# Kernel tuning notes

Hardware: AMD Instinct MI355X
Metric: run time of the kernel (lower is better)

The kernel has to match this reference:

```python
import jax, jax.numpy as jnp
import numpy as np

N = 50000            # nodes
E = 800000           # random edges (self loops added in reference, per PyG default)
D_IN, D1, D2, D_OUT = 256, 128, 64, 40
SLOPE = 0.2          # GATv2Conv default negative_slope


def _glorot(key, shape):
    fan_in, fan_out = shape[0], shape[-1]
    s = jnp.sqrt(6.0 / (fan_in + fan_out))
    return jax.random.uniform(key, shape, jnp.float32, -s, s)


def setup_inputs() -> dict:
    key = jax.random.key(0)
    ks = jax.random.split(key, 16)
    inp = {
        "x": jax.random.normal(ks[0], (N, D_IN), jnp.float32),
        "edge_index": jax.random.randint(ks[1], (2, E), 0, N),
    }
    dims = [(D_IN, D1), (D1, D2), (D2, D_OUT)]
    k = 2
    for i, (di, do) in enumerate(dims, 1):
        inp[f"W{i}l"] = _glorot(ks[k], (di, do)); k += 1
        inp[f"W{i}r"] = _glorot(ks[k], (di, do)); k += 1
        inp[f"b{i}l"] = jnp.zeros((do,), jnp.float32)
        inp[f"b{i}r"] = jnp.zeros((do,), jnp.float32)
        inp[f"a{i}"]  = _glorot(ks[k], (do,));    k += 1
        inp[f"c{i}"]  = jnp.zeros((do,), jnp.float32)
    return inp


def _gatv2(x, src, dst, Wl, bl, Wr, br, att, bias):
    # GATv2Conv, heads=1: lin_l on source nodes, lin_r on target nodes
    xl = x @ Wl + bl                     # [N, do] source transform
    xr = x @ Wr + br                     # [N, do] target transform
    e = jax.nn.leaky_relu(xl[src] + xr[dst], SLOPE)   # [Etot, do]
    logits = e @ att                     # [Etot]
    # segment softmax over incoming edges of each dst node
    m = jax.ops.segment_max(logits, dst, num_segments=N)
    ex = jnp.exp(logits - m[dst])
    denom = jax.ops.segment_sum(ex, dst, num_segments=N)
    alpha = ex / denom[dst]              # [Etot]
    out = jax.ops.segment_sum(alpha[:, None] * xl[src], dst, num_segments=N)
    return out + bias


def reference(x, edge_index,
              W1l, W1r, b1l, b1r, a1, c1,
              W2l, W2r, b2l, b2r, a2, c2,
              W3l, W3r, b3l, b3r, a3, c3):
    loop = jnp.arange(N, dtype=edge_index.dtype)
    src = jnp.concatenate([edge_index[0], loop])   # add_self_loops=True
    dst = jnp.concatenate([edge_index[1], loop])
    h = jax.nn.relu(_gatv2(x, src, dst, W1l, b1l, W1r, b1r, a1, c1))
    h = jax.nn.relu(_gatv2(h, src, dst, W2l, b2l, W2r, b2r, a2, c2))
    h = _gatv2(h, src, dst, W3l, b3l, W3r, b3r, a3, c3)
    return jax.nn.log_softmax(h, axis=1)
```

## Files before the change

### kernel.cpp

```cpp
#include <hip/hip_runtime.h>
#include <math.h>

#define NN 50000
#define NE 800000
#define SLOPE 0.2f
#define NEGX (-1e30f)
#define CH 8192

typedef _Float16 h8 __attribute__((ext_vector_type(8)));
typedef _Float16 h2 __attribute__((ext_vector_type(2)));
typedef float f8 __attribute__((ext_vector_type(8)));
typedef float v4f __attribute__((ext_vector_type(4)));

__device__ __forceinline__ h8 hzero(){ h8 z = {0,0,0,0,0,0,0,0}; return z; }

__device__ __forceinline__ void pack_one(const float* __restrict__ W,
                                         _Float16* __restrict__ Wp,
                                         int DO, int K, int NT, int t){
  int KC = K >> 5;
  if (t >= NT * KC * 64) return;
  int lane = t & 63;
  int rest = t >> 6;
  int c  = rest % KC;
  int nt = rest / KC;
  int col = nt * 16 + (lane & 15);
  int k0  = c * 32 + ((lane >> 4) << 3);
  _Float16 o[8];
#pragma unroll
  for (int j = 0; j < 8; j++){
    float v = (col < DO) ? W[(k0 + j) * DO + col] : 0.f;
    o[j] = (_Float16)v;
  }
  *(ulonglong2*)(Wp + (size_t)t * 8) = *(ulonglong2*)o;
}

__global__ __launch_bounds__(256) void k_pack_hist(
    const float* W1l, const float* W1r, const float* W2l,
    const float* W2r, const float* W3l, const float* W3r,
    _Float16* p1l, _Float16* p1r, _Float16* p2l,
    _Float16* p2r, _Float16* p3l, _Float16* p3r,
    const int* __restrict__ ei, int* __restrict__ gbp){
  __shared__ int h[256];
  int b = blockIdx.x, t = threadIdx.x;
  if (b < 44){
    if      (b < 16) pack_one(W1l, p1l, 128, 256, 8, (b     ) * 256 + t);
    else if (b < 32) pack_one(W1r, p1r, 128, 256, 8, (b - 16) * 256 + t);
    else if (b < 36) pack_one(W2l, p2l,  64, 128, 4, (b - 32) * 256 + t);
    else if (b < 40) pack_one(W2r, p2r,  64, 128, 4, (b - 36) * 256 + t);
    else if (b < 42) pack_one(W3l, p3l,  40,  64, 3, (b - 40) * 256 + t);
    else             pack_one(W3r, p3r,  40,  64, 3, (b - 42) * 256 + t);
  } else {
    int hb = b - 44;
    h[t] = 0;
    __syncthreads();
    int e0 = hb * 12500;
    for (int i = t; i < 12500; i += 256)
      atomicAdd(&h[ei[NE + e0 + i] >> 8], 1);
    __syncthreads();
    gbp[hb * 256 + t] = h[t];
  }
}

__global__ __launch_bounds__(256) void k_scan(const int* __restrict__ gbp,
                                              int* __restrict__ base,
                                              int* __restrict__ bcur,
                                              int* __restrict__ row_ptr){
  __shared__ int s[256];
  int t = threadIdx.x;
  int v = 0;
#pragma unroll 8
  for (int i = 0; i < 64; i++) v += gbp[i * 256 + t];
  s[t] = v; __syncthreads();
  for (int off = 1; off < 256; off <<= 1){
    int a = (t >= off) ? s[t - off] : 0;
    __syncthreads(); s[t] += a; __syncthreads();
  }
  int ex = s[t] - v;
  base[t] = ex;
  bcur[t] = ex;
  if (t == 255){ base[256] = s[255]; row_ptr[NN] = s[255]; }
}

__global__ __launch_bounds__(256) void k_bscatter(const int* __restrict__ ei,
                                                  int* __restrict__ bcur,
                                                  unsigned* __restrict__ pk_out){
  __shared__ unsigned pk[CH];
  __shared__ int h[256];
  int t = threadIdx.x;
  int e0 = blockIdx.x * CH;
  h[t] = 0;
  __syncthreads();
  int n = NE - e0; if (n > CH) n = CH;
  for (int i = t; i < n; i += 256){
    int e = e0 + i;
    int s = ei[e], d = ei[NE + e];
    pk[i] = (unsigned)s | ((unsigned)(d & 255) << 16) | ((unsigned)(d >> 8) << 24);
    atomicAdd(&h[d >> 8], 1);
  }
  __syncthreads();
  int c = h[t];
  if (c) h[t] = atomicAdd(&bcur[t], c);
  __syncthreads();
  for (int i = t; i < n; i += 256){
    unsigned u = pk[i];
    int pos = atomicAdd(&h[u >> 24], 1);
    pk_out[pos] = u;
  }
}

__global__ __launch_bounds__(256) void k_bcsr(const unsigned* __restrict__ pk,
                                              const int* __restrict__ base,
                                              int* __restrict__ row_ptr,
                                              int* __restrict__ csr_src){
  __shared__ int h[256], s[256];
  int t = threadIdx.x;
  int b = blockIdx.x;
  int lo = base[b], hi = base[b + 1];
  h[t] = 0;
  __syncthreads();
  for (int i = lo + t; i < hi; i += 256)
    atomicAdd(&h[(pk[i] >> 16) & 255], 1);
  __syncthreads();
  int v = h[t];
  s[t] = v; __syncthreads();
  for (int off = 1; off < 256; off <<= 1){
    int a = (t >= off) ? s[t - off] : 0;
    __syncthreads(); s[t] += a; __syncthreads();
  }
  int ex = lo + s[t] - v;
  int node = b * 256 + t;
  if (node < NN) row_ptr[node] = ex;
  h[t] = ex;
  __syncthreads();
  for (int i = lo + t; i < hi; i += 256){
    unsigned u = pk[i];
    int pos = atomicAdd(&h[(u >> 16) & 255], 1);
    csr_src[pos] = (int)(u & 0xFFFFu);
  }
}

template<typename TI, int K, int DO>
__global__ __launch_bounds__(256, 4) void gemm_direct(
    const TI* __restrict__ X,
    const _Float16* __restrict__ Wpl, const float* __restrict__ bl,
    const _Float16* __restrict__ Wpr, const float* __restrict__ br,
    _Float16* __restrict__ Yl, _Float16* __restrict__ Yr)
{
  constexpr int KC = K / 32;
  constexpr int NT = (DO + 15) / 16;
  int lane = threadIdx.x & 63;
  int wv   = threadIdx.x >> 6;
  int row0 = (blockIdx.x * 4 + wv) * 16;
  int arow = lane & 15;
  int koff = lane >> 4;
  int lrow = row0 + arow;
  int crow = (lrow < NN) ? lrow : 0;

  h8 afrag[KC];
  if constexpr (sizeof(TI) == 4){
    const float* Xr = (const float*)X + (size_t)crow * K + koff * 8;
#pragma unroll
    for (int c = 0; c < KC; c++){
      float4 v0 = *reinterpret_cast<const float4*>(Xr + c * 32);
      float4 v1 = *reinterpret_cast<const float4*>(Xr + c * 32 + 4);
      h8 a;
      a[0]=(_Float16)v0.x; a[1]=(_Float16)v0.y; a[2]=(_Float16)v0.z; a[3]=(_Float16)v0.w;
      a[4]=(_Float16)v1.x; a[5]=(_Float16)v1.y; a[6]=(_Float16)v1.z; a[7]=(_Float16)v1.w;
      afrag[c] = a;
    }
  } else {
    const _Float16* Xr = (const _Float16*)X + (size_t)crow * K + koff * 8;
#pragma unroll
    for (int c = 0; c < KC; c++)
      afrag[c] = *reinterpret_cast<const h8*>(Xr + c * 32);
  }

#pragma unroll
  for (int side = 0; side < 2; side++){
    const _Float16* Wp = side ? Wpr : Wpl;
    const float* bias = side ? br : bl;
    _Float16* Y = side ? Yr : Yl;
#pragma unroll
    for (int nt = 0; nt < NT; nt++){
      v4f acc = {0.f, 0.f, 0.f, 0.f};
#pragma unroll
      for (int c = 0; c < KC; c++){
        h8 b = *reinterpret_cast<const h8*>(Wp + (size_t)((nt * KC + c) * 64 + lane) * 8);
        acc = __builtin_amdgcn_mfma_f32_16x16x32_f16(afrag[c], b, acc, 0, 0, 0);
      }
      int col = nt * 16 + arow;
      if (col < DO){
        float bv = bias[col];
        int rbase = row0 + koff * 4;
#pragma unroll
        for (int r = 0; r < 4; r++){
          int orow = rbase + r;
          if (orow < NN) Y[(size_t)orow * DO + col] = (_Float16)(acc[r] + bv);
        }
      }
    }
  }
}

__device__ __forceinline__ float edge_logit(h8 x, h8 xrv, h8 attv){
  h8 t = x + xrv;
  h8 l = __builtin_elementwise_max(t, t * (_Float16)SLOPE);
  const h2* lp = (const h2*)&l;
  const h2* ap = (const h2*)&attv;
  h2 d = lp[0] * ap[0];
  d += lp[1] * ap[1];
  d += lp[2] * ap[2];
  d += lp[3] * ap[3];
  return (float)d[0] + (float)d[1];
}

template<int LPG>
__device__ __forceinline__ float gsum(float v){
#pragma unroll
  for (int off = 1; off < LPG; off <<= 1) v += __shfl_xor(v, off, 64);
  return v;
}
template<int LPG>
__device__ __forceinline__ void gsum2(float& a, float& b){
#pragma unroll
  for (int off = 1; off < LPG; off <<= 1){
    a += __shfl_xor(a, off, 64);
    b += __shfl_xor(b, off, 64);
  }
}
template<int LPG>
__device__ __forceinline__ float gmax(float v){
#pragma unroll
  for (int off = 1; off < LPG; off <<= 1) v = fmaxf(v, __shfl_xor(v, off, 64));
  return v;
}

template<int DO, int LPG, int DO2>
__global__ __launch_bounds__(256) void agg_gemm(
    const _Float16* __restrict__ xl, const _Float16* __restrict__ xr,
    const int* __restrict__ csr_src, const int* __restrict__ row_ptr,
    const float* __restrict__ att, const float* __restrict__ bias,
    const _Float16* __restrict__ Wpl2, const float* __restrict__ bl2,
    const _Float16* __restrict__ Wpr2, const float* __restrict__ br2,
    _Float16* __restrict__ Yl, _Float16* __restrict__ Yr)
{
  constexpr int G = 64 / LPG;
  constexpr int NPB = 4 * G;
  constexpr int LK = DO + 8;
  constexpr int KC2 = DO / 32;
  constexpr int NT2 = (DO2 + 15) / 16;
  constexpr int MT = NPB / 16;
  __shared__ _Float16 hs[NPB * LK];

  int lane = threadIdx.x & 63;
  int wid  = threadIdx.x >> 6;
  int g = lane / LPG, p = lane % LPG;
  int nodeLocal = wid * G + g;
  int node = blockIdx.x * NPB + nodeLocal;
  int cbase = p * 8;
  bool nvalid = node < NN;
  int nodeC = nvalid ? node : 0;

  h8 attv, xrv, xlv;
  {
    float4 a0 = *reinterpret_cast<const float4*>(att + cbase);
    float4 a1 = *reinterpret_cast<const float4*>(att + cbase + 4);
    attv[0]=(_Float16)a0.x; attv[1]=(_Float16)a0.y; attv[2]=(_Float16)a0.z; attv[3]=(_Float16)a0.w;
    attv[4]=(_Float16)a1.x; attv[5]=(_Float16)a1.y; attv[6]=(_Float16)a1.z; attv[7]=(_Float16)a1.w;
    xrv = *reinterpret_cast<const h8*>(xr + nodeC * DO + cbase);
    xlv = *reinterpret_cast<const h8*>(xl + nodeC * DO + cbase);
  }
  float s = gsum<LPG>(edge_logit(xlv, xrv, attv));
  float wS = __expf(s);
  float denA = wS, denB = 0.f;
  float accA[8], accB[8];
  {
    f8 xf = __builtin_convertvector(xlv, f8);
#pragma unroll
    for (int j = 0; j < 8; j++){ accA[j] = wS * xf[j]; accB[j] = 0.f; }
  }

  int e0 = row_ptr[nodeC];
  int e1 = nvalid ? row_ptr[nodeC + 1] : e0;
  int e = e0;
  for (; e + 1 < e1; e += 2){
    int sA = csr_src[e], sB = csr_src[e + 1];
    h8 xA = *reinterpret_cast<const h8*>(xl + sA * DO + cbase);
    h8 xB = *reinterpret_cast<const h8*>(xl + sB * DO + cbase);
    float pA = edge_logit(xA, xrv, attv);
    float pB = edge_logit(xB, xrv, attv);
    gsum2<LPG>(pA, pB);
    float wA = __expf(pA), wB = __expf(pB);
    denA += wA; denB += wB;
    f8 fA = __builtin_convertvector(xA, f8);
    f8 fB = __builtin_convertvector(xB, f8);
#pragma unroll
    for (int j = 0; j < 8; j++){
      accA[j] = fmaf(wA, fA[j], accA[j]);
      accB[j] = fmaf(wB, fB[j], accB[j]);
    }
  }
  if (e < e1){
    int sA = csr_src[e];
    h8 xA = *reinterpret_cast<const h8*>(xl + sA * DO + cbase);
    float pA = gsum<LPG>(edge_logit(xA, xrv, attv));
    float w = __expf(pA);
    denA += w;
    f8 fA = __builtin_convertvector(xA, f8);
#pragma unroll
    for (int j = 0; j < 8; j++) accA[j] = fmaf(w, fA[j], accA[j]);
  }

  {
    float inv = 1.0f / (denA + denB);
    f8 vv;
#pragma unroll
    for (int j = 0; j < 8; j++)
      vv[j] = fmaxf(fmaf(accA[j] + accB[j], inv, bias[cbase + j]), 0.f);
    h8 ho = __builtin_convertvector(vv, h8);
    *reinterpret_cast<h8*>(&hs[nodeLocal * LK + cbase]) = ho;
  }
  __syncthreads();

  int arow = lane & 15;
  int koff = lane >> 4;
  int mt = (MT == 1) ? 0 : (wid >> 1);
  h8 afrag[KC2];
#pragma unroll
  for (int c = 0; c < KC2; c++)
    afrag[c] = *reinterpret_cast<const h8*>(&hs[(mt * 16 + arow) * LK + koff * 8 + c * 32]);

  int row0 = blockIdx.x * NPB + mt * 16;
  int side = wid & 1;
  const _Float16* Wp = side ? Wpr2 : Wpl2;
  const float* bias2 = side ? br2 : bl2;
  _Float16* Y = side ? Yr : Yl;
  int nt_begin = (MT == 1) ? (wid >> 1) * (NT2 / 2) : 0;
  int nt_end   = (MT == 1) ? nt_begin + NT2 / 2 : NT2;
  for (int nt = nt_begin; nt < nt_end; nt++){
    v4f acc = {0.f, 0.f, 0.f, 0.f};
#pragma unroll
    for (int c = 0; c < KC2; c++){
      h8 b = *reinterpret_cast<const h8*>(Wp + (size_t)((nt * KC2 + c) * 64 + lane) * 8);
      acc = __builtin_amdgcn_mfma_f32_16x16x32_f16(afrag[c], b, acc, 0, 0, 0);
    }
    int col = nt * 16 + arow;
    if (col < DO2){
      float bv = bias2[col];
      int rbase = row0 + koff * 4;
#pragma unroll
      for (int r = 0; r < 4; r++){
        int orow = rbase + r;
        if (orow < NN) Y[(size_t)orow * DO2 + col] = (_Float16)(acc[r] + bv);
      }
    }
  }
}

template<int DO, int LPG>
__global__ __launch_bounds__(256) void gat_agg_out(
    const _Float16* __restrict__ xl, const _Float16* __restrict__ xr,
    const int* __restrict__ csr_src, const int* __restrict__ row_ptr,
    const float* __restrict__ att, const float* __restrict__ bias,
    float* __restrict__ out)
{
  constexpr int G = 64 / LPG;
  int lane = threadIdx.x & 63;
  int wv = (blockIdx.x * 256 + threadIdx.x) >> 6;
  int g = lane / LPG;
  int p = lane % LPG;
  int node = wv * G + g;
  if (node >= NN) return;
  int cbase = p * 8;
  bool ok = (cbase < DO);

  h8 attv = hzero(), xrv = hzero(), xlv = hzero();
  if (ok){
    float4 a0 = *reinterpret_cast<const float4*>(att + cbase);
    float4 a1 = *reinterpret_cast<const float4*>(att + cbase + 4);
    attv[0]=(_Float16)a0.x; attv[1]=(_Float16)a0.y; attv[2]=(_Float16)a0.z; attv[3]=(_Float16)a0.w;
    attv[4]=(_Float16)a1.x; attv[5]=(_Float16)a1.y; attv[6]=(_Float16)a1.z; attv[7]=(_Float16)a1.w;
    xrv = *reinterpret_cast<const h8*>(xr + node * DO + cbase);
    xlv = *reinterpret_cast<const h8*>(xl + node * DO + cbase);
  }

  float s = gsum<LPG>(edge_logit(xlv, xrv, attv));
  float wS = __expf(s);
  float denA = wS, denB = 0.f;
  float accA[8], accB[8];
  {
    f8 xf = __builtin_convertvector(xlv, f8);
#pragma unroll
    for (int j = 0; j < 8; j++){ accA[j] = wS * xf[j]; accB[j] = 0.f; }
  }

  int e0 = row_ptr[node], e1 = row_ptr[node + 1];
  int e = e0;
  for (; e + 1 < e1; e += 2){
    int sA = csr_src[e], sB = csr_src[e + 1];
    h8 xA = ok ? *reinterpret_cast<const h8*>(xl + sA * DO + cbase) : hzero();
    h8 xB = ok ? *reinterpret_cast<const h8*>(xl + sB * DO + cbase) : hzero();
    float pA = edge_logit(xA, xrv, attv);
    float pB = edge_logit(xB, xrv, attv);
    gsum2<LPG>(pA, pB);
    float wA = __expf(pA), wB = __expf(pB);
    denA += wA; denB += wB;
    f8 fA = __builtin_convertvector(xA, f8);
    f8 fB = __builtin_convertvector(xB, f8);
#pragma unroll
    for (int j = 0; j < 8; j++){
      accA[j] = fmaf(wA, fA[j], accA[j]);
      accB[j] = fmaf(wB, fB[j], accB[j]);
    }
  }
  if (e < e1){
    int sA = csr_src[e];
    h8 xA = ok ? *reinterpret_cast<const h8*>(xl + sA * DO + cbase) : hzero();
    float pA = gsum<LPG>(edge_logit(xA, xrv, attv));
    float w = __expf(pA);
    denA += w;
    f8 fA = __builtin_convertvector(xA, f8);
#pragma unroll
    for (int j = 0; j < 8; j++) accA[j] = fmaf(w, fA[j], accA[j]);
  }

  float inv = 1.0f / (denA + denB);
  float v[8]; float lmax = NEGX;
#pragma unroll
  for (int j = 0; j < 8; j++){
    v[j] = ok ? fmaf(accA[j] + accB[j], inv, bias[cbase + j]) : NEGX;
    lmax = fmaxf(lmax, v[j]);
  }
  lmax = gmax<LPG>(lmax);
  float lsum = 0.f;
#pragma unroll
  for (int j = 0; j < 8; j++) lsum += __expf(v[j] - lmax);
  lsum = gsum<LPG>(lsum);
  if (ok){
    float lg = lmax + __logf(lsum);
    float* op = (float*)out + node * DO + cbase;
    float4 o0, o1;
    o0.x = v[0] - lg; o0.y = v[1] - lg; o0.z = v[2] - lg; o0.w = v[3] - lg;
    o1.x = v[4] - lg; o1.y = v[5] - lg; o1.z = v[6] - lg; o1.w = v[7] - lg;
    *reinterpret_cast<float4*>(op) = o0;
    *reinterpret_cast<float4*>(op + 4) = o1;
  }
}

extern "C" void kernel_launch(void* const* d_in, const int* in_sizes, int n_in,
                              void* d_out, int out_size, void* d_ws, size_t ws_size,
                              hipStream_t stream) {
  const float* x   = (const float*)d_in[0];
  const int*   ei  = (const int*)d_in[1];
  const float* W1l = (const float*)d_in[2];  const float* W1r = (const float*)d_in[3];
  const float* b1l = (const float*)d_in[4];  const float* b1r = (const float*)d_in[5];
  const float* a1  = (const float*)d_in[6];  const float* c1  = (const float*)d_in[7];
  const float* W2l = (const float*)d_in[8];  const float* W2r = (const float*)d_in[9];
  const float* b2l = (const float*)d_in[10]; const float* b2r = (const float*)d_in[11];
  const float* a2  = (const float*)d_in[12]; const float* c2  = (const float*)d_in[13];
  const float* W3l = (const float*)d_in[14]; const float* W3r = (const float*)d_in[15];
  const float* b3l = (const float*)d_in[16]; const float* b3r = (const float*)d_in[17];
  const float* a3  = (const float*)d_in[18]; const float* c3  = (const float*)d_in[19];
  float* outp = (float*)d_out;

  _Float16* xl1 = (_Float16*)d_ws;
  _Float16* xr1 = xl1 + 6400000;
  _Float16* xl2 = xr1 + 6400000;
  _Float16* xr2 = xl2 + 3200000;
  _Float16* xl3 = xr2 + 3200000;
  _Float16* xr3 = xl3 + 2000000;
  _Float16* wp1l = xr3 + 2000000;
  _Float16* wp1r = wp1l + 32768;
  _Float16* wp2l = wp1r + 32768;
  _Float16* wp2r = wp2l + 8192;
  _Float16* wp3l = wp2r + 8192;
  _Float16* wp3r = wp3l + 3072;
  unsigned* pk   = (unsigned*)(wp3r + 3072);
  int* csr_src   = (int*)(pk + NE);
  int* row_ptr   = csr_src + NE;
  int* gbp       = row_ptr + 50001;
  int* base      = gbp + 16384;
  int* bcur      = base + 257;

  const int GB = (NN + 63) / 64;
  const int SB = (NE + CH - 1) / CH;
  const int FB1 = (NN + 15) / 16;
  const int FB2 = (NN + 31) / 32;
  const int AB3 = (NN + 31) / 32;

  k_pack_hist<<<108, 256, 0, stream>>>(W1l, W1r, W2l, W2r, W3l, W3r,
                                       wp1l, wp1r, wp2l, wp2r, wp3l, wp3r,
                                       ei, gbp);
  k_scan<<<1, 256, 0, stream>>>(gbp, base, bcur, row_ptr);
  k_bscatter<<<SB, 256, 0, stream>>>(ei, bcur, pk);
  k_bcsr<<<196, 256, 0, stream>>>(pk, base, row_ptr, csr_src);

  gemm_direct<float,256,128><<<GB, 256, 0, stream>>>(x, wp1l, b1l, wp1r, b1r, xl1, xr1);

  agg_gemm<128,16,64><<<FB1, 256, 0, stream>>>(xl1, xr1, csr_src, row_ptr,
                                               a1, c1, wp2l, b2l, wp2r, b2r, xl2, xr2);

  agg_gemm<64,8,40><<<FB2, 256, 0, stream>>>(xl2, xr2, csr_src, row_ptr,
                                             a2, c2, wp3l, b3l, wp3r, b3r, xl3, xr3);

  gat_agg_out<40,8><<<AB3, 256, 0, stream>>>(xl3, xr3, csr_src, row_ptr, a3, c3, outp);
}
```

Baseline: 285.6 us.

## Sort nodes by degree within each block and unroll edge loop by four

Each block now computes its nodes' in-degrees, ranks them in shared memory, and assigns nodes to wave groups in degree order, so the groups within a wave have similar edge counts and less divergence. The GEMM epilogue writes rows through the resulting permutation. The edge loop gains a 4-way unrolled path with batched shuffle reductions to keep more gathers in flight, and the accumulators become vector types. It costs extra syncthreads, an O(NPB^2) ranking step and scattered row writes.

```diff
diff --git a/kernel.cpp b/kernel.cpp
--- a/kernel.cpp
+++ b/kernel.cpp
@@ -13,6 +13,7 @@
 typedef float v4f __attribute__((ext_vector_type(4)));
 
 __device__ __forceinline__ h8 hzero(){ h8 z = {0,0,0,0,0,0,0,0}; return z; }
+__device__ __forceinline__ f8 fzero(){ f8 z = {0,0,0,0,0,0,0,0}; return z; }
 
 __device__ __forceinline__ void pack_one(const float* __restrict__ W,
                                          _Float16* __restrict__ Wp,
@@ -229,6 +230,16 @@
   }
 }
 template<int LPG>
+__device__ __forceinline__ void gsum4(float& a, float& b, float& c, float& d){
+#pragma unroll
+  for (int off = 1; off < LPG; off <<= 1){
+    a += __shfl_xor(a, off, 64);
+    b += __shfl_xor(b, off, 64);
+    c += __shfl_xor(c, off, 64);
+    d += __shfl_xor(d, off, 64);
+  }
+}
+template<int LPG>
 __device__ __forceinline__ float gmax(float v){
 #pragma unroll
   for (int off = 1; off < LPG; off <<= 1) v = fmaxf(v, __shfl_xor(v, off, 64));
@@ -251,12 +262,33 @@
   constexpr int NT2 = (DO2 + 15) / 16;
   constexpr int MT = NPB / 16;
   __shared__ _Float16 hs[NPB * LK];
-
-  int lane = threadIdx.x & 63;
-  int wid  = threadIdx.x >> 6;
+  __shared__ int nodeOf[NPB];
+  __shared__ int degOf[NPB];
+
+  int tid  = threadIdx.x;
+  int lane = tid & 63;
+  int wid  = tid >> 6;
+
+  if (tid < NPB){
+    int nd = blockIdx.x * NPB + tid;
+    degOf[tid] = (nd < NN) ? (row_ptr[nd + 1] - row_ptr[nd]) : -1;
+  }
+  __syncthreads();
+  if (tid < NPB){
+    int dg = degOf[tid];
+    int r = 0;
+#pragma unroll
+    for (int j = 0; j < NPB; j++){
+      int dj = degOf[j];
+      r += (dj < dg) || (dj == dg && j < tid);
+    }
+    nodeOf[r] = blockIdx.x * NPB + tid;
+  }
+  __syncthreads();
+
   int g = lane / LPG, p = lane % LPG;
   int nodeLocal = wid * G + g;
-  int node = blockIdx.x * NPB + nodeLocal;
+  int node = nodeOf[nodeLocal];
   int cbase = p * 8;
   bool nvalid = node < NN;
   int nodeC = nvalid ? node : 0;
@@ -273,16 +305,36 @@
   float s = gsum<LPG>(edge_logit(xlv, xrv, attv));
   float wS = __expf(s);
   float denA = wS, denB = 0.f;
-  float accA[8], accB[8];
+  f8 accA, accB;
   {
     f8 xf = __builtin_convertvector(xlv, f8);
-#pragma unroll
-    for (int j = 0; j < 8; j++){ accA[j] = wS * xf[j]; accB[j] = 0.f; }
+    accA = xf * wS;
+    accB = fzero();
   }
 
   int e0 = row_ptr[nodeC];
   int e1 = nvalid ? row_ptr[nodeC + 1] : e0;
   int e = e0;
+  for (; e + 3 < e1; e += 4){
+    int s0 = csr_src[e],     s1 = csr_src[e + 1];
+    int s2 = csr_src[e + 2], s3 = csr_src[e + 3];
+    h8 x0 = *reinterpret_cast<const h8*>(xl + s0 * DO + cbase);
+    h8 x1 = *reinterpret_cast<const h8*>(xl + s1 * DO + cbase);
+    h8 x2 = *reinterpret_cast<const h8*>(xl + s2 * DO + cbase);
+    h8 x3 = *reinterpret_cast<const h8*>(xl + s3 * DO + cbase);
+    float p0 = edge_logit(x0, xrv, attv);
+    float p1 = edge_logit(x1, xrv, attv);
+    float p2 = edge_logit(x2, xrv, attv);
+    float p3 = edge_logit(x3, xrv, attv);
+    gsum4<LPG>(p0, p1, p2, p3);
+    float w0 = __expf(p0), w1 = __expf(p1);
+    float w2 = __expf(p2), w3 = __expf(p3);
+    denA += w0 + w2; denB += w1 + w3;
+    accA = __builtin_convertvector(x0, f8) * w0 + accA;
+    accB = __builtin_convertvector(x1, f8) * w1 + accB;
+    accA = __builtin_convertvector(x2, f8) * w2 + accA;
+    accB = __builtin_convertvector(x3, f8) * w3 + accB;
+  }
   for (; e + 1 < e1; e += 2){
     int sA = csr_src[e], sB = csr_src[e + 1];
     h8 xA = *reinterpret_cast<const h8*>(xl + sA * DO + cbase);
@@ -292,13 +344,8 @@
     gsum2<LPG>(pA, pB);
     float wA = __expf(pA), wB = __expf(pB);
     denA += wA; denB += wB;
-    f8 fA = __builtin_convertvector(xA, f8);
-    f8 fB = __builtin_convertvector(xB, f8);
-#pragma unroll
-    for (int j = 0; j < 8; j++){
-      accA[j] = fmaf(wA, fA[j], accA[j]);
-      accB[j] = fmaf(wB, fB[j], accB[j]);
-    }
+    accA = __builtin_convertvector(xA, f8) * wA + accA;
+    accB = __builtin_convertvector(xB, f8) * wB + accB;
   }
   if (e < e1){
     int sA = csr_src[e];
@@ -306,19 +353,18 @@
     float pA = gsum<LPG>(edge_logit(xA, xrv, attv));
     float w = __expf(pA);
     denA += w;
-    f8 fA = __builtin_convertvector(xA, f8);
-#pragma unroll
-    for (int j = 0; j < 8; j++) accA[j] = fmaf(w, fA[j], accA[j]);
+    accA = __builtin_convertvector(xA, f8) * w + accA;
   }
 
   {
     float inv = 1.0f / (denA + denB);
-    f8 vv;
-#pragma unroll
-    for (int j = 0; j < 8; j++)
-      vv[j] = fmaxf(fmaf(accA[j] + accB[j], inv, bias[cbase + j]), 0.f);
-    h8 ho = __builtin_convertvector(vv, h8);
-    *reinterpret_cast<h8*>(&hs[nodeLocal * LK + cbase]) = ho;
+    f8 sum = (accA + accB) * inv;
+    float4 b0 = *reinterpret_cast<const float4*>(bias + cbase);
+    float4 b1 = *reinterpret_cast<const float4*>(bias + cbase + 4);
+    f8 bv = {b0.x, b0.y, b0.z, b0.w, b1.x, b1.y, b1.z, b1.w};
+    sum += bv;
+    sum = __builtin_elementwise_max(sum, fzero());
+    *reinterpret_cast<h8*>(&hs[nodeLocal * LK + cbase]) = __builtin_convertvector(sum, h8);
   }
   __syncthreads();
 
@@ -330,7 +376,6 @@
   for (int c = 0; c < KC2; c++)
     afrag[c] = *reinterpret_cast<const h8*>(&hs[(mt * 16 + arow) * LK + koff * 8 + c * 32]);
 
-  int row0 = blockIdx.x * NPB + mt * 16;
   int side = wid & 1;
   const _Float16* Wp = side ? Wpr2 : Wpl2;
   const float* bias2 = side ? br2 : bl2;
@@ -347,10 +392,10 @@
     int col = nt * 16 + arow;
     if (col < DO2){
       float bv = bias2[col];
-      int rbase = row0 + koff * 4;
+      int lrbase = mt * 16 + koff * 4;
 #pragma unroll
       for (int r = 0; r < 4; r++){
-        int orow = rbase + r;
+        int orow = nodeOf[lrbase + r];
         if (orow < NN) Y[(size_t)orow * DO2 + col] = (_Float16)(acc[r] + bv);
       }
     }
@@ -365,12 +410,35 @@
     float* __restrict__ out)
 {
   constexpr int G = 64 / LPG;
-  int lane = threadIdx.x & 63;
-  int wv = (blockIdx.x * 256 + threadIdx.x) >> 6;
+  constexpr int NPB = 4 * G;
+  __shared__ int nodeOf[NPB];
+  __shared__ int degOf[NPB];
+  int tid  = threadIdx.x;
+  int lane = tid & 63;
+  int wid  = tid >> 6;
+
+  if (tid < NPB){
+    int nd = blockIdx.x * NPB + tid;
+    degOf[tid] = (nd < NN) ? (row_ptr[nd + 1] - row_ptr[nd]) : -1;
+  }
+  __syncthreads();
+  if (tid < NPB){
+    int dg = degOf[tid];
+    int r = 0;
+#pragma unroll
+    for (int j = 0; j < NPB; j++){
+      int dj = degOf[j];
+      r += (dj < dg) || (dj == dg && j < tid);
+    }
+    nodeOf[r] = blockIdx.x * NPB + tid;
+  }
+  __syncthreads();
+
   int g = lane / LPG;
   int p = lane % LPG;
-  int node = wv * G + g;
-  if (node >= NN) return;
+  int node = nodeOf[wid * G + g];
+  bool nvalid = node < NN;
+  int nodeC = nvalid ? node : 0;
   int cbase = p * 8;
   bool ok = (cbase < DO);
 
@@ -380,22 +448,43 @@
     float4 a1 = *reinterpret_cast<const float4*>(att + cbase + 4);
     attv[0]=(_Float16)a0.x; attv[1]=(_Float16)a0.y; attv[2]=(_Float16)a0.z; attv[3]=(_Float16)a0.w;
     attv[4]=(_Float16)a1.x; attv[5]=(_Float16)a1.y; attv[6]=(_Float16)a1.z; attv[7]=(_Float16)a1.w;
-    xrv = *reinterpret_cast<const h8*>(xr + node * DO + cbase);
-    xlv = *reinterpret_cast<const h8*>(xl + node * DO + cbase);
+    xrv = *reinterpret_cast<const h8*>(xr + nodeC * DO + cbase);
+    xlv = *reinterpret_cast<const h8*>(xl + nodeC * DO + cbase);
   }
 
   float s = gsum<LPG>(edge_logit(xlv, xrv, attv));
   float wS = __expf(s);
   float denA = wS, denB = 0.f;
-  float accA[8], accB[8];
+  f8 accA, accB;
   {
     f8 xf = __builtin_convertvector(xlv, f8);
-#pragma unroll
-    for (int j = 0; j < 8; j++){ accA[j] = wS * xf[j]; accB[j] = 0.f; }
-  }
-
-  int e0 = row_ptr[node], e1 = row_ptr[node + 1];
+    accA = xf * wS;
+    accB = fzero();
+  }
+
+  int e0 = row_ptr[nodeC];
+  int e1 = nvalid ? row_ptr[nodeC + 1] : e0;
   int e = e0;
+  for (; e + 3 < e1; e += 4){
+    int s0 = csr_src[e],     s1 = csr_src[e + 1];
+    int s2 = csr_src[e + 2], s3 = csr_src[e + 3];
+    h8 x0 = ok ? *reinterpret_cast<const h8*>(xl + s0 * DO + cbase) : hzero();
+    h8 x1 = ok ? *reinterpret_cast<const h8*>(xl + s1 * DO + cbase) : hzero();
+    h8 x2 = ok ? *reinterpret_cast<const h8*>(xl + s2 * DO + cbase) : hzero();
+    h8 x3 = ok ? *reinterpret_cast<const h8*>(xl + s3 * DO + cbase) : hzero();
+    float p0 = edge_logit(x0, xrv, attv);
+    float p1 = edge_logit(x1, xrv, attv);
+    float p2 = edge_logit(x2, xrv, attv);
+    float p3 = edge_logit(x3, xrv, attv);
+    gsum4<LPG>(p0, p1, p2, p3);
+    float w0 = __expf(p0), w1 = __expf(p1);
+    float w2 = __expf(p2), w3 = __expf(p3);
+    denA += w0 + w2; denB += w1 + w3;
+    accA = __builtin_convertvector(x0, f8) * w0 + accA;
+    accB = __builtin_convertvector(x1, f8) * w1 + accB;
+    accA = __builtin_convertvector(x2, f8) * w2 + accA;
+    accB = __builtin_convertvector(x3, f8) * w3 + accB;
+  }
   for (; e + 1 < e1; e += 2){
     int sA = csr_src[e], sB = csr_src[e + 1];
     h8 xA = ok ? *reinterpret_cast<const h8*>(xl + sA * DO + cbase) : hzero();
@@ -405,13 +494,8 @@
     gsum2<LPG>(pA, pB);
     float wA = __expf(pA), wB = __expf(pB);
     denA += wA; denB += wB;
-    f8 fA = __builtin_convertvector(xA, f8);
-    f8 fB = __builtin_convertvector(xB, f8);
-#pragma unroll
-    for (int j = 0; j < 8; j++){
-      accA[j] = fmaf(wA, fA[j], accA[j]);
-      accB[j] = fmaf(wB, fB[j], accB[j]);
-    }
+    accA = __builtin_convertvector(xA, f8) * wA + accA;
+    accB = __builtin_convertvector(xB, f8) * wB + accB;
   }
   if (e < e1){
     int sA = csr_src[e];
@@ -419,16 +503,15 @@
     float pA = gsum<LPG>(edge_logit(xA, xrv, attv));
     float w = __expf(pA);
     denA += w;
-    f8 fA = __builtin_convertvector(xA, f8);
-#pragma unroll
-    for (int j = 0; j < 8; j++) accA[j] = fmaf(w, fA[j], accA[j]);
+    accA = __builtin_convertvector(xA, f8) * w + accA;
   }
 
   float inv = 1.0f / (denA + denB);
+  f8 sumv = (accA + accB) * inv;
   float v[8]; float lmax = NEGX;
 #pragma unroll
   for (int j = 0; j < 8; j++){
-    v[j] = ok ? fmaf(accA[j] + accB[j], inv, bias[cbase + j]) : NEGX;
+    v[j] = ok ? (sumv[j] + bias[cbase + j]) : NEGX;
     lmax = fmaxf(lmax, v[j]);
   }
   lmax = gmax<LPG>(lmax);
@@ -436,7 +519,7 @@
 #pragma unroll
   for (int j = 0; j < 8; j++) lsum += __expf(v[j] - lmax);
   lsum = gsum<LPG>(lsum);
-  if (ok){
+  if (ok && nvalid){
     float lg = lmax + __logf(lsum);
     float* op = (float*)out + node * DO + cbase;
     float4 o0, o1;
```

After: 290.1 us. Within noise of the previous version (+1.6%).

## Software-pipeline edge gathers in 4-edge batches with index prefetch

Applied to the files above, without the earlier changes.

Restructures the per-node edge aggregation loop in both aggregation kernels to process four edges per step. It prefetches the next batch's feature rows and the following batch's CSR indices while the current batch is being computed, using masked clamped indices instead of remainder handling. The goal is to raise memory-level parallelism on the irregular gathers and hide their latency. It also adds a launch-bounds occupancy hint and vectorises the accumulators and bias epilogue. The deeper pipeline raises register pressure, and short-degree nodes do wasted work on masked lanes.

```diff
diff --git a/kernel.cpp b/kernel.cpp
--- a/kernel.cpp
+++ b/kernel.cpp
@@ -13,6 +13,7 @@
 typedef float v4f __attribute__((ext_vector_type(4)));
 
 __device__ __forceinline__ h8 hzero(){ h8 z = {0,0,0,0,0,0,0,0}; return z; }
+__device__ __forceinline__ f8 fzero(){ f8 z = {0,0,0,0,0,0,0,0}; return z; }
 
 __device__ __forceinline__ void pack_one(const float* __restrict__ W,
                                          _Float16* __restrict__ Wp,
@@ -221,11 +222,13 @@
   return v;
 }
 template<int LPG>
-__device__ __forceinline__ void gsum2(float& a, float& b){
+__device__ __forceinline__ void gsum4(float& a, float& b, float& c, float& d){
 #pragma unroll
   for (int off = 1; off < LPG; off <<= 1){
     a += __shfl_xor(a, off, 64);
     b += __shfl_xor(b, off, 64);
+    c += __shfl_xor(c, off, 64);
+    d += __shfl_xor(d, off, 64);
   }
 }
 template<int LPG>
@@ -236,7 +239,7 @@
 }
 
 template<int DO, int LPG, int DO2>
-__global__ __launch_bounds__(256) void agg_gemm(
+__global__ __launch_bounds__(256, 4) void agg_gemm(
     const _Float16* __restrict__ xl, const _Float16* __restrict__ xr,
     const int* __restrict__ csr_src, const int* __restrict__ row_ptr,
     const float* __restrict__ att, const float* __restrict__ bias,
@@ -273,52 +276,84 @@
   float s = gsum<LPG>(edge_logit(xlv, xrv, attv));
   float wS = __expf(s);
   float denA = wS, denB = 0.f;
-  float accA[8], accB[8];
+  f8 accA, accB;
   {
     f8 xf = __builtin_convertvector(xlv, f8);
-#pragma unroll
-    for (int j = 0; j < 8; j++){ accA[j] = wS * xf[j]; accB[j] = 0.f; }
+    accA = xf * wS;
+    accB = fzero();
   }
 
   int e0 = row_ptr[nodeC];
   int e1 = nvalid ? row_ptr[nodeC + 1] : e0;
-  int e = e0;
-  for (; e + 1 < e1; e += 2){
-    int sA = csr_src[e], sB = csr_src[e + 1];
-    h8 xA = *reinterpret_cast<const h8*>(xl + sA * DO + cbase);
-    h8 xB = *reinterpret_cast<const h8*>(xl + sB * DO + cbase);
-    float pA = edge_logit(xA, xrv, attv);
-    float pB = edge_logit(xB, xrv, attv);
-    gsum2<LPG>(pA, pB);
-    float wA = __expf(pA), wB = __expf(pB);
-    denA += wA; denB += wB;
-    f8 fA = __builtin_convertvector(xA, f8);
-    f8 fB = __builtin_convertvector(xB, f8);
-#pragma unroll
-    for (int j = 0; j < 8; j++){
-      accA[j] = fmaf(wA, fA[j], accA[j]);
-      accB[j] = fmaf(wB, fB[j], accB[j]);
-    }
-  }
-  if (e < e1){
-    int sA = csr_src[e];
-    h8 xA = *reinterpret_cast<const h8*>(xl + sA * DO + cbase);
-    float pA = gsum<LPG>(edge_logit(xA, xrv, attv));
-    float w = __expf(pA);
-    denA += w;
-    f8 fA = __builtin_convertvector(xA, f8);
-#pragma unroll
-    for (int j = 0; j < 8; j++) accA[j] = fmaf(w, fA[j], accA[j]);
+  int deg = e1 - e0;
+  int clampE = (deg > 0) ? e1 - 1 : 0;
+
+  if (deg > 0){
+    int ic[4]; float vc[4]; h8 xc[4];
+#pragma unroll
+    for (int k = 0; k < 4; k++){
+      int ee = e0 + k; bool v = ee < e1;
+      ic[k] = csr_src[v ? ee : clampE]; vc[k] = v ? 1.f : 0.f;
+    }
+#pragma unroll
+    for (int k = 0; k < 4; k++)
+      xc[k] = *reinterpret_cast<const h8*>(xl + ic[k] * DO + cbase);
+    int in_[4]; float vn[4];
+    if (deg > 4){
+#pragma unroll
+      for (int k = 0; k < 4; k++){
+        int ee = e0 + 4 + k; bool v = ee < e1;
+        in_[k] = csr_src[v ? ee : clampE]; vn[k] = v ? 1.f : 0.f;
+      }
+    }
+    int i = 0;
+    while (true){
+      bool more = (i + 4 < deg);
+      h8 xn[4];
+      if (more){
+#pragma unroll
+        for (int k = 0; k < 4; k++)
+          xn[k] = *reinterpret_cast<const h8*>(xl + in_[k] * DO + cbase);
+      }
+      bool more2 = (i + 8 < deg);
+      int i2[4]; float v2[4];
+      if (more2){
+#pragma unroll
+        for (int k = 0; k < 4; k++){
+          int ee = e0 + i + 8 + k; bool v = ee < e1;
+          i2[k] = csr_src[v ? ee : clampE]; v2[k] = v ? 1.f : 0.f;
+        }
+      }
+      float p0 = edge_logit(xc[0], xrv, attv);
+      float p1 = edge_logit(xc[1], xrv, attv);
+      float p2 = edge_logit(xc[2], xrv, attv);
+      float p3 = edge_logit(xc[3], xrv, attv);
+      gsum4<LPG>(p0, p1, p2, p3);
+      float w0 = __expf(p0) * vc[0], w1 = __expf(p1) * vc[1];
+      float w2 = __expf(p2) * vc[2], w3 = __expf(p3) * vc[3];
+      denA += w0 + w2; denB += w1 + w3;
+      accA = __builtin_convertvector(xc[0], f8) * w0 + accA;
+      accB = __builtin_convertvector(xc[1], f8) * w1 + accB;
+      accA = __builtin_convertvector(xc[2], f8) * w2 + accA;
+      accB = __builtin_convertvector(xc[3], f8) * w3 + accB;
+      if (!more) break;
+#pragma unroll
+      for (int k = 0; k < 4; k++){
+        xc[k] = xn[k]; vc[k] = vn[k]; in_[k] = i2[k]; vn[k] = v2[k];
+      }
+      i += 4;
+    }
   }
 
   {
     float inv = 1.0f / (denA + denB);
-    f8 vv;
-#pragma unroll
-    for (int j = 0; j < 8; j++)
-      vv[j] = fmaxf(fmaf(accA[j] + accB[j], inv, bias[cbase + j]), 0.f);
-    h8 ho = __builtin_convertvector(vv, h8);
-    *reinterpret_cast<h8*>(&hs[nodeLocal * LK + cbase]) = ho;
+    f8 sum = (accA + accB) * inv;
+    float4 b0 = *reinterpret_cast<const float4*>(bias + cbase);
+    float4 b1 = *reinterpret_cast<const float4*>(bias + cbase + 4);
+    f8 bv = {b0.x, b0.y, b0.z, b0.w, b1.x, b1.y, b1.z, b1.w};
+    sum += bv;
+    sum = __builtin_elementwise_max(sum, fzero());
+    *reinterpret_cast<h8*>(&hs[nodeLocal * LK + cbase]) = __builtin_convertvector(sum, h8);
   }
   __syncthreads();
 
@@ -358,7 +393,7 @@
 }
 
 template<int DO, int LPG>
-__global__ __launch_bounds__(256) void gat_agg_out(
+__global__ __launch_bounds__(256, 4) void gat_agg_out(
     const _Float16* __restrict__ xl, const _Float16* __restrict__ xr,
     const int* __restrict__ csr_src, const int* __restrict__ row_ptr,
     const float* __restrict__ att, const float* __restrict__ bias,
@@ -387,48 +422,80 @@
   float s = gsum<LPG>(edge_logit(xlv, xrv, attv));
   float wS = __expf(s);
   float denA = wS, denB = 0.f;
-  float accA[8], accB[8];
+  f8 accA, accB;
   {
     f8 xf = __builtin_convertvector(xlv, f8);
-#pragma unroll
-    for (int j = 0; j < 8; j++){ accA[j] = wS * xf[j]; accB[j] = 0.f; }
+    accA = xf * wS;
+    accB = fzero();
   }
 
   int e0 = row_ptr[node], e1 = row_ptr[node + 1];
-  int e = e0;
-  for (; e + 1 < e1; e += 2){
-    int sA = csr_src[e], sB = csr_src[e + 1];
-    h8 xA = ok ? *reinterpret_cast<const h8*>(xl + sA * DO + cbase) : hzero();
-    h8 xB = ok ? *reinterpret_cast<const h8*>(xl + sB * DO + cbase) : hzero();
-    float pA = edge_logit(xA, xrv, attv);
-    float pB = edge_logit(xB, xrv, attv);
-    gsum2<LPG>(pA, pB);
-    float wA = __expf(pA), wB = __expf(pB);
-    denA += wA; denB += wB;
-    f8 fA = __builtin_convertvector(xA, f8);
-    f8 fB = __builtin_convertvector(xB, f8);
-#pragma unroll
-    for (int j = 0; j < 8; j++){
-      accA[j] = fmaf(wA, fA[j], accA[j]);
-      accB[j] = fmaf(wB, fB[j], accB[j]);
-    }
-  }
-  if (e < e1){
-    int sA = csr_src[e];
-    h8 xA = ok ? *reinterpret_cast<const h8*>(xl + sA * DO + cbase) : hzero();
-    float pA = gsum<LPG>(edge_logit(xA, xrv, attv));
-    float w = __expf(pA);
-    denA += w;
-    f8 fA = __builtin_convertvector(xA, f8);
-#pragma unroll
-    for (int j = 0; j < 8; j++) accA[j] = fmaf(w, fA[j], accA[j]);
+  int deg = e1 - e0;
+  int clampE = (deg > 0) ? e1 - 1 : 0;
+
+  if (deg > 0){
+    int ic[4]; float vc[4]; h8 xc[4];
+#pragma unroll
+    for (int k = 0; k < 4; k++){
+      int ee = e0 + k; bool v = ee < e1;
+      ic[k] = csr_src[v ? ee : clampE]; vc[k] = v ? 1.f : 0.f;
+    }
+#pragma unroll
+    for (int k = 0; k < 4; k++)
+      xc[k] = ok ? *reinterpret_cast<const h8*>(xl + ic[k] * DO + cbase) : hzero();
+    int in_[4]; float vn[4];
+    if (deg > 4){
+#pragma unroll
+      for (int k = 0; k < 4; k++){
+        int ee = e0 + 4 + k; bool v = ee < e1;
+        in_[k] = csr_src[v ? ee : clampE]; vn[k] = v ? 1.f : 0.f;
+      }
+    }
+    int i = 0;
+    while (true){
+      bool more = (i + 4 < deg);
+      h8 xn[4];
+      if (more){
+#pragma unroll
+        for (int k = 0; k < 4; k++)
+          xn[k] = ok ? *reinterpret_cast<const h8*>(xl + in_[k] * DO + cbase) : hzero();
+      }
+      bool more2 = (i + 8 < deg);
+      int i2[4]; float v2[4];
+      if (more2){
+#pragma unroll
+        for (int k = 0; k < 4; k++){
+          int ee = e0 + i + 8 + k; bool v = ee < e1;
+          i2[k] = csr_src[v ? ee : clampE]; v2[k] = v ? 1.f : 0.f;
+        }
+      }
+      float p0 = edge_logit(xc[0], xrv, attv);
+      float p1 = edge_logit(xc[1], xrv, attv);
+      float p2 = edge_logit(xc[2], xrv, attv);
+      float p3 = edge_logit(xc[3], xrv, attv);
+      gsum4<LPG>(p0, p1, p2, p3);
+      float w0 = __expf(p0) * vc[0], w1 = __expf(p1) * vc[1];
+      float w2 = __expf(p2) * vc[2], w3 = __expf(p3) * vc[3];
+      denA += w0 + w2; denB += w1 + w3;
+      accA = __builtin_convertvector(xc[0], f8) * w0 + accA;
+      accB = __builtin_convertvector(xc[1], f8) * w1 + accB;
+      accA = __builtin_convertvector(xc[2], f8) * w2 + accA;
+      accB = __builtin_convertvector(xc[3], f8) * w3 + accB;
+      if (!more) break;
+#pragma unroll
+      for (int k = 0; k < 4; k++){
+        xc[k] = xn[k]; vc[k] = vn[k]; in_[k] = i2[k]; vn[k] = v2[k];
+      }
+      i += 4;
+    }
   }
 
   float inv = 1.0f / (denA + denB);
+  f8 sumv = (accA + accB) * inv;
   float v[8]; float lmax = NEGX;
 #pragma unroll
   for (int j = 0; j < 8; j++){
-    v[j] = ok ? fmaf(accA[j] + accB[j], inv, bias[cbase + j]) : NEGX;
+    v[j] = ok ? (sumv[j] + bias[cbase + j]) : NEGX;
     lmax = fmaxf(lmax, v[j]);
   }
   lmax = gmax<LPG>(lmax);
```

After: 300.7 us. 1.05x slower.
